# Optimization experiments

Hardware: AMD Instinct MI355X
Metric: run time of the kernel (lower is better)

The kernel has to match this reference:

```python
import jax, jax.numpy as jnp
import numpy as np

B = 1024      # molecules (segments)
K = 16        # conformers per molecule
N = B * K     # total nodes
C = 128       # in_out_dimension
HID = 256     # hidden_dimension of gate MLP
HEADS = 2
LAYERS = 2


def _leaky(x, slope):
    return jnp.where(x >= 0, x, slope * x)


def setup_inputs() -> dict:
    key = jax.random.key(0)
    ks = jax.random.split(key, 12)
    # segment ids: K conformers per molecule, sorted
    batch = jnp.repeat(jnp.arange(B, dtype=jnp.int64), K)
    # fully connected within each segment, no self loops, then append self loops
    idx = np.arange(N, dtype=np.int64).reshape(B, K)
    src = np.broadcast_to(idx[:, :, None], (B, K, K)).reshape(-1)
    dst = np.broadcast_to(idx[:, None, :], (B, K, K)).reshape(-1)
    keep = src != dst
    e_src = jnp.asarray(np.concatenate([src[keep], np.arange(N, dtype=np.int64)]))
    e_dst = jnp.asarray(np.concatenate([dst[keep], np.arange(N, dtype=np.int64)]))
    sc = 1.0 / np.sqrt(C)
    sh = 1.0 / np.sqrt(HID)
    inp = {
        "H": jax.random.normal(ks[0], (N, C), jnp.float32),
        "batch": batch,
        "edge_src": e_src,
        "edge_dst": e_dst,
        "Wl": jax.random.normal(ks[1], (LAYERS, C, HEADS * C), jnp.float32) * sc,
        "bl": jnp.zeros((LAYERS, HEADS * C), jnp.float32),
        "Wr": jax.random.normal(ks[2], (LAYERS, C, HEADS * C), jnp.float32) * sc,
        "br": jnp.zeros((LAYERS, HEADS * C), jnp.float32),
        "att": jax.random.normal(ks[3], (LAYERS, HEADS, C), jnp.float32) * sc,
        "gat_bias": jnp.zeros((LAYERS, C), jnp.float32),
        "gW1": jax.random.normal(ks[4], (C, HID), jnp.float32) * sc,
        "gb1": jnp.zeros((HID,), jnp.float32),
        "gW2": jax.random.normal(ks[5], (HID, HID), jnp.float32) * sh,
        "gb2": jnp.zeros((HID,), jnp.float32),
        "gW3": jax.random.normal(ks[6], (HID, 1), jnp.float32) * sh,
        "gb3": jnp.zeros((1,), jnp.float32),
    }
    return inp


def _segment_softmax(logits, seg, num_segments):
    m = jax.ops.segment_max(logits, seg, num_segments=num_segments)
    ex = jnp.exp(logits - m[seg])
    den = jax.ops.segment_sum(ex, seg, num_segments=num_segments)
    return ex / den[seg]


def _gatv2(x, e_src, e_dst, Wl, bl, Wr, br, att, bias):
    # GATv2Conv, concat=False (mean over heads), negative_slope=0.2
    xl = (x @ Wl + bl).reshape(N, HEADS, C)   # source transform
    xr = (x @ Wr + br).reshape(N, HEADS, C)   # target transform
    e = _leaky(xl[e_src] + xr[e_dst], 0.2)    # [E, H, C]
    logits = jnp.einsum('ehc,hc->eh', e, att) # [E, H]
    alpha = _segment_softmax(logits, e_dst, N)
    out = jax.ops.segment_sum(xl[e_src] * alpha[:, :, None], e_dst, num_segments=N)
    return out.mean(axis=1) + bias            # [N, C]


def reference(H, batch, edge_src, edge_dst, Wl, bl, Wr, br, att, gat_bias,
              gW1, gb1, gW2, gb2, gW3, gb3):
    x = H
    for l in range(LAYERS):
        x = _gatv2(x, edge_src, edge_dst, Wl[l], bl[l], Wr[l], br[l], att[l], gat_bias[l])
    # gate MLP (LeakyReLU default slope 0.01)
    h = _leaky(x @ gW1 + gb1, 0.01)
    h = _leaky(h @ gW2 + gb2, 0.01)
    h_gate = h @ gW3 + gb3                    # [N, 1]
    scores = _segment_softmax(h_gate, batch, B)
    h_pool = jax.ops.segment_sum(x * scores, batch, num_segments=B)  # [B, C]
    return (h_pool, scores)
```

## Files before the change

### kernel.cpp

```cpp
#include <hip/hip_runtime.h>
#include <hip/hip_bf16.h>
#include <math.h>

#define N_NODES 16384
#define B_MOL   1024

typedef __attribute__((ext_vector_type(8))) short short8v;
typedef __attribute__((ext_vector_type(4))) float f32x4;

static __device__ __forceinline__ unsigned short f2bf(float f) {
    unsigned int u = __float_as_uint(f);
    unsigned int r = (u + 0x7FFFu + ((u >> 16) & 1u)) >> 16;
    return (unsigned short)r;
}
static __device__ __forceinline__ float bf2f(unsigned short h) {
    return __uint_as_float(((unsigned int)h) << 16);
}

__global__ __launch_bounds__(256)
void conv_pack(const float* __restrict__ Wl, const float* __restrict__ Wr,
               const float* __restrict__ g1, const float* __restrict__ g2,
               unsigned short* __restrict__ wpk) {
    int idx = blockIdx.x * 256 + threadIdx.x;
    if (idx >= 229376) return;
    float v; size_t base; int nK, k, col;
    if (idx < 131072) {
        int l = idx >> 16;
        int e = idx & 65535;
        k = e >> 9; col = e & 511;
        v = (col < 256) ? Wl[l * 32768 + k * 256 + col]
                        : Wr[l * 32768 + k * 256 + (col - 256)];
        base = (size_t)l * 131072; nK = 4;
    } else if (idx < 163840) {
        int e = idx - 131072; k = e >> 8; col = e & 255;
        v = g1[k * 256 + col]; base = 262144; nK = 4;
    } else {
        int e = idx - 163840; k = e >> 8; col = e & 255;
        v = g2[k * 256 + col]; base = 327680; nK = 8;
    }
    int cb = col >> 4, ci = col & 15, ks = k >> 5, kk = k & 31;
    int lane = ((kk >> 3) << 4) | ci;
    size_t fo = ((size_t)(cb * nK + ks) * 2) * 512 + lane * 8 + (kk & 7);
    unsigned short h = f2bf(v);
    wpk[base + fo] = h;
    wpk[base + fo + 512] = f2bf(v - bf2f(h));
}

template<int NK, int NCB>
static __device__ __forceinline__ void tile_gemm16(
        const short* __restrict__ Ah, const short* __restrict__ Al,
        const unsigned short* __restrict__ wv,
        f32x4 (&acc)[NCB], int lane) {
    int lr = lane & 15;
    int kq = (lane >> 4) * 8;
    short8v bc[NCB][2], bn[NCB][2];
    #pragma unroll
    for (int j = 0; j < NCB; ++j) {
        bc[j][0] = *(const short8v*)&wv[((j * NK + 0) * 2 + 0) * 512 + lane * 8];
        bc[j][1] = *(const short8v*)&wv[((j * NK + 0) * 2 + 1) * 512 + lane * 8];
    }
    #pragma unroll
    for (int ks = 0; ks < NK; ++ks) {
        if (ks + 1 < NK) {
            #pragma unroll
            for (int j = 0; j < NCB; ++j) {
                bn[j][0] = *(const short8v*)&wv[((j * NK + ks + 1) * 2 + 0) * 512 + lane * 8];
                bn[j][1] = *(const short8v*)&wv[((j * NK + ks + 1) * 2 + 1) * 512 + lane * 8];
            }
        }
        int ro = lr * 264 + ks * 32 + kq;
        short8v ah = *(const short8v*)&Ah[ro];
        short8v al = *(const short8v*)&Al[ro];
        #pragma unroll
        for (int j = 0; j < NCB; ++j)
            acc[j] = __builtin_amdgcn_mfma_f32_16x16x32_bf16(ah, bc[j][0], acc[j], 0, 0, 0);
        #pragma unroll
        for (int j = 0; j < NCB; ++j)
            acc[j] = __builtin_amdgcn_mfma_f32_16x16x32_bf16(ah, bc[j][1], acc[j], 0, 0, 0);
        #pragma unroll
        for (int j = 0; j < NCB; ++j)
            acc[j] = __builtin_amdgcn_mfma_f32_16x16x32_bf16(al, bc[j][0], acc[j], 0, 0, 0);
        if (ks + 1 < NK) {
            #pragma unroll
            for (int j = 0; j < NCB; ++j) { bc[j][0] = bn[j][0]; bc[j][1] = bn[j][1]; }
        }
    }
}

static __device__ __forceinline__ void pack_pair(f32x4 o, short4* ph, short4* pl) {
    unsigned short h0 = f2bf(o[0]), h1 = f2bf(o[1]), h2 = f2bf(o[2]), h3 = f2bf(o[3]);
    *ph = make_short4((short)h0, (short)h1, (short)h2, (short)h3);
    *pl = make_short4((short)f2bf(o[0] - bf2f(h0)), (short)f2bf(o[1] - bf2f(h1)),
                      (short)f2bf(o[2] - bf2f(h2)), (short)f2bf(o[3] - bf2f(h3)));
}

__global__ __launch_bounds__(512, 4)
void mega(const float* __restrict__ H, const unsigned short* __restrict__ wpk,
          const float* __restrict__ bl, const float* __restrict__ br,
          const float* __restrict__ att, const float* __restrict__ gbias,
          const float* __restrict__ gb1, const float* __restrict__ gb2,
          const float* __restrict__ gW3, const float* __restrict__ gb3,
          float* __restrict__ out) {
    __shared__ short sAh[16][264], sAl[16][264];
    __shared__ float sL[16][260], sR[16][260];
    __shared__ float sLog[32][20];
    __shared__ float sAtt[512];
    __shared__ float sg[16], ssc[16];

    int tid  = threadIdx.x;
    int lane = tid & 63;
    int w    = tid >> 6;
    int lr   = lane & 15;
    int mol  = blockIdx.x;
    int rowBase = mol * 16;

    {
        int r = tid >> 5, q = tid & 31;
        f32x4 v = *(const f32x4*)&H[(size_t)(rowBase + r) * 128 + q * 4];
        pack_pair(v, (short4*)&sAh[r][q * 4], (short4*)&sAl[r][q * 4]);
        sAtt[tid] = att[tid];
    }
    __syncthreads();

    for (int l = 0; l < 2; ++l) {
        {
            #pragma unroll
            for (int p = 0; p < 2; ++p) {
                f32x4 acc[2];
                acc[0] = (f32x4){0.f, 0.f, 0.f, 0.f};
                acc[1] = (f32x4){0.f, 0.f, 0.f, 0.f};
                int cb0 = w * 4 + p * 2;
                tile_gemm16<4, 2>(&sAh[0][0], &sAl[0][0],
                                  wpk + (size_t)l * 131072 + (size_t)cb0 * 4096,
                                  acc, lane);
                float* dst; int cbase; const float* bp;
                if (w < 4) { dst = &sL[0][0]; cbase = w * 64 + p * 32; bp = bl + l * 256; }
                else       { dst = &sR[0][0]; cbase = (w - 4) * 64 + p * 32; bp = br + l * 256; }
                int row0 = (lane >> 4) * 4;
                #pragma unroll
                for (int j = 0; j < 2; ++j) {
                    int cl = cbase + j * 16 + lr;
                    float bv = bp[cl];
                    #pragma unroll
                    for (int t = 0; t < 4; ++t)
                        dst[(row0 + t) * 260 + cl] = acc[j][t] + bv;
                }
            }
        }
        __syncthreads();

        {
            int dh  = tid >> 4;
            int s   = tid & 15;
            int d   = dh >> 1, hh = dh & 1;
            const float* xrp = &sR[d][hh * 128];
            const float* xlp = &sL[s][hh * 128];
            const float* ap  = &sAtt[l * 256 + hh * 128];
            float ac = 0.f;
            #pragma unroll 8
            for (int c4 = 0; c4 < 32; ++c4) {
                f32x4 av = *(const f32x4*)&ap[c4 * 4];
                f32x4 xv = *(const f32x4*)&xlp[c4 * 4];
                f32x4 rv = *(const f32x4*)&xrp[c4 * 4];
                f32x4 e = xv + rv;
                ac += 0.6f * av[0] * e[0] + 0.4f * av[0] * fabsf(e[0])
                    + 0.6f * av[1] * e[1] + 0.4f * av[1] * fabsf(e[1])
                    + 0.6f * av[2] * e[2] + 0.4f * av[2] * fabsf(e[2])
                    + 0.6f * av[3] * e[3] + 0.4f * av[3] * fabsf(e[3]);
            }
            float mx = ac;
            #pragma unroll
            for (int off = 1; off < 16; off <<= 1)
                mx = fmaxf(mx, __shfl_xor(mx, off, 16));
            float e = expf(ac - mx);
            float den = e;
            #pragma unroll
            for (int off = 1; off < 16; off <<= 1)
                den += __shfl_xor(den, off, 16);
            sLog[dh][s] = e / den;
        }
        __syncthreads();

        {
            int d  = tid >> 5;
            int cw = tid & 31;
            f32x4 f0 = (f32x4){0.f, 0.f, 0.f, 0.f};
            #pragma unroll
            for (int hh = 0; hh < 2; ++hh) {
                const float* alr = &sLog[d * 2 + hh][0];
                #pragma unroll
                for (int s = 0; s < 16; ++s) {
                    int se = (s + 2 * cw) & 15;
                    f0 += alr[se] * *(const f32x4*)&sL[se][hh * 128 + cw * 4];
                }
            }
            f32x4 o = f0 * 0.5f + *(const f32x4*)&gbias[l * 128 + cw * 4];
            pack_pair(o, (short4*)&sAh[d][cw * 4], (short4*)&sAl[d][cw * 4]);
            if (l == 1)
                *(f32x4*)&sR[d][128 + cw * 4] = o;
        }
        __syncthreads();
    }

    {
        f32x4 acc[2];
        acc[0] = (f32x4){0.f, 0.f, 0.f, 0.f};
        acc[1] = (f32x4){0.f, 0.f, 0.f, 0.f};
        tile_gemm16<4, 2>(&sAh[0][0], &sAl[0][0],
                          wpk + 262144 + (size_t)w * 8192, acc, lane);
        __syncthreads();
        int row0 = (lane >> 4) * 4;
        #pragma unroll
        for (int j = 0; j < 2; ++j) {
            int cl = w * 32 + j * 16 + lr;
            float bv = gb1[cl];
            #pragma unroll
            for (int t = 0; t < 4; ++t) {
                float v = acc[j][t] + bv;
                v = v >= 0.f ? v : 0.01f * v;
                unsigned short h = f2bf(v);
                sAh[row0 + t][cl] = (short)h;
                sAl[row0 + t][cl] = (short)f2bf(v - bf2f(h));
            }
        }
    }
    __syncthreads();

    {
        f32x4 acc[2];
        acc[0] = (f32x4){0.f, 0.f, 0.f, 0.f};
        acc[1] = (f32x4){0.f, 0.f, 0.f, 0.f};
        tile_gemm16<8, 2>(&sAh[0][0], &sAl[0][0],
                          wpk + 327680 + (size_t)w * 16384, acc, lane);
        int row0 = (lane >> 4) * 4;
        #pragma unroll
        for (int j = 0; j < 2; ++j) {
            int cl = w * 32 + j * 16 + lr;
            float bv = gb2[cl];
            #pragma unroll
            for (int t = 0; t < 4; ++t) {
                float v = acc[j][t] + bv;
                v = v >= 0.f ? v : 0.01f * v;
                sL[row0 + t][cl] = v;
            }
        }
    }
    __syncthreads();

    {
        int grow = tid >> 5, l32 = tid & 31;
        f32x4 h2a = *(const f32x4*)&sL[grow][l32 * 8];
        f32x4 h2b = *(const f32x4*)&sL[grow][l32 * 8 + 4];
        f32x4 w3a = *(const f32x4*)&gW3[l32 * 8];
        f32x4 w3b = *(const f32x4*)&gW3[l32 * 8 + 4];
        float p = h2a[0] * w3a[0] + h2a[1] * w3a[1] + h2a[2] * w3a[2] + h2a[3] * w3a[3]
                + h2b[0] * w3b[0] + h2b[1] * w3b[1] + h2b[2] * w3b[2] + h2b[3] * w3b[3];
        #pragma unroll
        for (int off = 16; off; off >>= 1) p += __shfl_down(p, off, 32);
        if (l32 == 0) sg[grow] = p + gb3[0];
    }
    __syncthreads();

    if (tid < 16) {
        float v = sg[tid];
        float mx = v;
        #pragma unroll
        for (int off = 8; off; off >>= 1) mx = fmaxf(mx, __shfl_xor(mx, off, 16));
        float e = expf(v - mx);
        float den = e;
        #pragma unroll
        for (int off = 8; off; off >>= 1) den += __shfl_xor(den, off, 16);
        float sc = e / den;
        ssc[tid] = sc;
        out[131072 + rowBase + tid] = sc;
    }
    __syncthreads();

    if (tid < 128) {
        float a = 0.f;
        #pragma unroll
        for (int s = 0; s < 16; ++s)
            a += ssc[s] * sR[s][128 + tid];
        out[(size_t)mol * 128 + tid] = a;
    }
}

extern "C" void kernel_launch(void* const* d_in, const int* in_sizes, int n_in,
                              void* d_out, int out_size, void* d_ws, size_t ws_size,
                              hipStream_t stream) {
    (void)in_sizes; (void)n_in; (void)out_size; (void)ws_size;
    const float* H        = (const float*)d_in[0];
    const float* Wl       = (const float*)d_in[4];
    const float* bl       = (const float*)d_in[5];
    const float* Wr       = (const float*)d_in[6];
    const float* br       = (const float*)d_in[7];
    const float* att      = (const float*)d_in[8];
    const float* gat_bias = (const float*)d_in[9];
    const float* gW1      = (const float*)d_in[10];
    const float* gb1      = (const float*)d_in[11];
    const float* gW2      = (const float*)d_in[12];
    const float* gb2      = (const float*)d_in[13];
    const float* gW3      = (const float*)d_in[14];
    const float* gb3      = (const float*)d_in[15];
    float* out = (float*)d_out;

    unsigned short* wpk = (unsigned short*)d_ws;

    conv_pack<<<896, 256, 0, stream>>>(Wl, Wr, gW1, gW2, wpk);
    mega<<<B_MOL, 512, 0, stream>>>(H, wpk, bl, br, att, gat_bias,
                                    gb1, gb2, gW3, gb3, out);
}
```

Before: 82.15 us.

## Register-tile GATv2 attention logits and move segment softmax into aggregation

The attention-logit stage now gives each thread a 4x4 block of (dst, src) pairs over a slice of channels, so every loaded xl/xr vector from shared memory is reused four times. Partial sums are reduced with 16-lane shuffles and raw logits are written to shared memory. The softmax (max, exp, normalise) is recomputed per thread inside the aggregation stage. Launch bounds drop the minimum occupancy hint from 4 to 1 to give the larger register tile room, at the risk of lower occupancy and redundant exp work.

After: 127.8 us. 55.6% more time.

```diff
diff --git a/kernel.cpp b/kernel.cpp
--- a/kernel.cpp
+++ b/kernel.cpp
@@ -94,7 +94,7 @@
                       (short)f2bf(o[2] - bf2f(h2)), (short)f2bf(o[3] - bf2f(h3)));
 }
 
-__global__ __launch_bounds__(512, 4)
+__global__ __launch_bounds__(512, 1)
 void mega(const float* __restrict__ H, const unsigned short* __restrict__ wpk,
           const float* __restrict__ bl, const float* __restrict__ br,
           const float* __restrict__ att, const float* __restrict__ gbias,
@@ -150,34 +150,50 @@
         __syncthreads();
 
         {
-            int dh  = tid >> 4;
-            int s   = tid & 15;
-            int d   = dh >> 1, hh = dh & 1;
-            const float* xrp = &sR[d][hh * 128];
-            const float* xlp = &sL[s][hh * 128];
-            const float* ap  = &sAtt[l * 256 + hh * 128];
-            float ac = 0.f;
-            #pragma unroll 8
-            for (int c4 = 0; c4 < 32; ++c4) {
-                f32x4 av = *(const f32x4*)&ap[c4 * 4];
-                f32x4 xv = *(const f32x4*)&xlp[c4 * 4];
-                f32x4 rv = *(const f32x4*)&xrp[c4 * 4];
-                f32x4 e = xv + rv;
-                ac += 0.6f * av[0] * e[0] + 0.4f * av[0] * fabsf(e[0])
-                    + 0.6f * av[1] * e[1] + 0.4f * av[1] * fabsf(e[1])
-                    + 0.6f * av[2] * e[2] + 0.4f * av[2] * fabsf(e[2])
-                    + 0.6f * av[3] * e[3] + 0.4f * av[3] * fabsf(e[3]);
-            }
-            float mx = ac;
-            #pragma unroll
-            for (int off = 1; off < 16; off <<= 1)
-                mx = fmaxf(mx, __shfl_xor(mx, off, 16));
-            float e = expf(ac - mx);
-            float den = e;
-            #pragma unroll
-            for (int off = 1; off < 16; off <<= 1)
-                den += __shfl_xor(den, off, 16);
-            sLog[dh][s] = e / den;
+            int hh = tid >> 8;
+            int db = (tid >> 6) & 3;
+            int sb = (tid >> 4) & 3;
+            int cq = tid & 15;
+            float ac[4][4];
+            #pragma unroll
+            for (int di = 0; di < 4; ++di)
+                #pragma unroll
+                for (int si = 0; si < 4; ++si) ac[di][si] = 0.f;
+            #pragma unroll
+            for (int t = 0; t < 2; ++t) {
+                int c4 = cq + 16 * t;
+                f32x4 av = *(const f32x4*)&sAtt[l * 256 + hh * 128 + c4 * 4];
+                f32x4 a6 = av * 0.6f, a4 = av * 0.4f;
+                f32x4 xrv[4], xlv[4];
+                #pragma unroll
+                for (int di = 0; di < 4; ++di)
+                    xrv[di] = *(const f32x4*)&sR[db * 4 + di][hh * 128 + c4 * 4];
+                #pragma unroll
+                for (int si = 0; si < 4; ++si)
+                    xlv[si] = *(const f32x4*)&sL[sb * 4 + si][hh * 128 + c4 * 4];
+                #pragma unroll
+                for (int di = 0; di < 4; ++di)
+                    #pragma unroll
+                    for (int si = 0; si < 4; ++si) {
+                        f32x4 e = xlv[si] + xrv[di];
+                        ac[di][si] += a6[0] * e[0] + a4[0] * fabsf(e[0])
+                                    + a6[1] * e[1] + a4[1] * fabsf(e[1])
+                                    + a6[2] * e[2] + a4[2] * fabsf(e[2])
+                                    + a6[3] * e[3] + a4[3] * fabsf(e[3]);
+                    }
+            }
+            #pragma unroll
+            for (int di = 0; di < 4; ++di)
+                #pragma unroll
+                for (int si = 0; si < 4; ++si) {
+                    float v = ac[di][si];
+                    v += __shfl_down(v, 8, 16);
+                    v += __shfl_down(v, 4, 16);
+                    v += __shfl_down(v, 2, 16);
+                    v += __shfl_down(v, 1, 16);
+                    if (cq == 0)
+                        sLog[(db * 4 + di) * 2 + hh][sb * 4 + si] = v;
+                }
         }
         __syncthreads();
 
@@ -187,11 +203,19 @@
             f32x4 f0 = (f32x4){0.f, 0.f, 0.f, 0.f};
             #pragma unroll
             for (int hh = 0; hh < 2; ++hh) {
-                const float* alr = &sLog[d * 2 + hh][0];
+                const float* lg = &sLog[d * 2 + hh][0];
+                float mx = lg[0];
+                #pragma unroll
+                for (int s = 1; s < 16; ++s) mx = fmaxf(mx, lg[s]);
+                float al[16];
+                float den = 0.f;
+                #pragma unroll
+                for (int s = 0; s < 16; ++s) { al[s] = expf(lg[s] - mx); den += al[s]; }
+                float inv = 1.f / den;
                 #pragma unroll
                 for (int s = 0; s < 16; ++s) {
                     int se = (s + 2 * cw) & 15;
-                    f0 += alr[se] * *(const f32x4*)&sL[se][hh * 128 + cw * 4];
+                    f0 += (al[se] * inv) * *(const f32x4*)&sL[se][hh * 128 + cw * 4];
                 }
             }
             f32x4 o = f0 * 0.5f + *(const f32x4*)&gbias[l * 128 + cw * 4];
```
